# Kernel tuning notes

Measured on AMD Instinct MI355X. Metric: run time of the kernel, lower is better.

The kernel has to match this reference:

```python
import jax, jax.numpy as jnp
import numpy as np

EMBED = 64
TEMPERATURE = 8.0
LN_EPS = 1e-6


def setup_inputs() -> dict:
    key = jax.random.key(0)
    ks = jax.random.split(key, 9)
    n_map, n_obs = 16384, 8192
    s = 1.0 / np.sqrt(EMBED)
    return {
        "map_code": jax.random.normal(ks[0], (n_map, EMBED), jnp.float32),
        "obs_code": jax.random.normal(ks[1], (n_obs, EMBED), jnp.float32),
        "Wq": jax.random.normal(ks[2], (EMBED, EMBED), jnp.float32) * s,
        "Wk": jax.random.normal(ks[3], (EMBED, EMBED), jnp.float32) * s,
        "Wv": jax.random.normal(ks[4], (EMBED, EMBED), jnp.float32) * s,
        "Wo": jax.random.normal(ks[5], (EMBED // 2, EMBED), jnp.float32) * (1.0 / np.sqrt(EMBED // 2)),
        "bo": jnp.zeros((EMBED,), jnp.float32),
        "gamma": jnp.ones((EMBED,), jnp.float32),
        "beta": jnp.zeros((EMBED,), jnp.float32),
    }


def _glu(x):
    a, b = jnp.split(x, 2, axis=-1)
    return a * jax.nn.sigmoid(b)


def reference(map_code, obs_code, Wq, Wk, Wv, Wo, bo, gamma, beta):
    # projections (x @ W == torch Linear with weight W.T; params are random either way)
    map_q = map_code @ Wq          # [Nm, E]
    map_k = map_code @ Wk          # [Nm, E]
    map_v = map_code @ Wv          # [Nm, E]
    obs_k = obs_code @ Wk          # [No, E]
    obs_v = obs_code @ Wv          # [No, E]

    self_score = jnp.sum(map_q * map_k, axis=-1, keepdims=True)   # [Nm, 1]
    obs_score = map_q @ obs_k.T                                   # [Nm, No]
    w = jax.nn.softmax(
        jnp.concatenate([self_score, obs_score], axis=-1) / TEMPERATURE,
        axis=-1,
    )  # [Nm, 1+No]

    # GLU gating: glu(obs_v) is identical for every map row, so the original's
    # [Nm, 1+No, E] broadcast collapses to a rank-2 contraction.
    gated_map = _glu(map_v)   # [Nm, E/2]
    gated_obs = _glu(obs_v)   # [No, E/2]
    agg = w[:, :1] * gated_map + w[:, 1:] @ gated_obs   # [Nm, E/2]

    out = agg @ Wo + bo + map_code   # [Nm, E]
    mu = jnp.mean(out, axis=-1, keepdims=True)
    var = jnp.mean(jnp.square(out - mu), axis=-1, keepdims=True)
    return (out - mu) * jax.lax.rsqrt(var + LN_EPS) * gamma + beta
```

## Files before the change

### kernel.cpp

```cpp
#include <hip/hip_runtime.h>
#include <hip/hip_bf16.h>


typedef float f32x16 __attribute__((ext_vector_type(16)));
typedef short bf16x8 __attribute__((ext_vector_type(8)));
typedef unsigned int u32;

__device__ __forceinline__ u32 cvt_pk_bf16(float lo, float hi) {
    u32 r;
    asm("v_cvt_pk_bf16_f32 %0, %1, %2" : "=v"(r) : "v"(lo), "v"(hi));
    return r;
}
__device__ __forceinline__ void permswap32(u32& a, u32& b) {
    asm("v_permlane32_swap_b32 %0, %1" : "+v"(a), "+v"(b));
}

#define IT 0.18033688011112042f
#define LOG2E 1.44269504089f

__global__ __launch_bounds__(256) void prep_kernel(
    const float* __restrict__ map_code, const float* __restrict__ obs_code,
    const float* __restrict__ Wq, const float* __restrict__ Wk,
    const float* __restrict__ Wv,
    __hip_bfloat16* __restrict__ qbf, __hip_bfloat16* __restrict__ Kp,
    __hip_bfloat16* __restrict__ Vp, float* __restrict__ self_score,
    float* __restrict__ gated_map, int n_map, int n_obs)
{
    __shared__ float xs[32 * 64];
    const int t = threadIdx.x;
    const int w = t >> 6;
    const int e = t & 63;
    const int r0 = blockIdx.x * 32;
    const int total = n_map + n_obs;

    #pragma unroll
    for (int i = 0; i < 8; ++i) {
        const int idx = i * 256 + t;
        const int gr = r0 + (idx >> 6);
        const int col = idx & 63;
        float val = 0.0f;
        if (gr < n_map)      val = map_code[(size_t)gr * 64 + col];
        else if (gr < total) val = obs_code[(size_t)(gr - n_map) * 64 + col];
        xs[idx] = val;
    }
    __syncthreads();

    float qa[8] = {}, ka[8] = {}, va[8] = {};
    const float* xw = xs + (w * 8) * 64;
    for (int d = 0; d < 64; ++d) {
        const float wq = Wq[d * 64 + e];
        const float wk = Wk[d * 64 + e];
        const float wv = Wv[d * 64 + e];
        #pragma unroll
        for (int i = 0; i < 8; ++i) {
            const float x = xw[i * 64 + d];
            qa[i] = fmaf(x, wq, qa[i]);
            ka[i] = fmaf(x, wk, ka[i]);
            va[i] = fmaf(x, wv, va[i]);
        }
    }

    #pragma unroll
    for (int i = 0; i < 8; ++i) {
        const int r = r0 + w * 8 + i;
        if (r >= total) break;
        const bool is_map = r < n_map;
        const float vother = __shfl_xor(va[i], 32);
        const float sig = 1.0f / (1.0f + __builtin_amdgcn_exp2f(-vother * LOG2E));
        const float g = va[i] * sig;

        if (is_map) {
            qbf[(size_t)r * 64 + e] = __float2bfloat16(qa[i] * IT);
            float qk = qa[i] * ka[i];
            #pragma unroll
            for (int off = 32; off; off >>= 1) qk += __shfl_xor(qk, off);
            if (e == 0) self_score[r] = qk;
            if (e < 32) gated_map[(size_t)r * 32 + e] = g;
        } else {
            const int j  = r - n_map;
            const int kb = j >> 5, jq = j & 31;
            {
                const int c = e >> 4, h2 = (e >> 3) & 1, ii = e & 7;
                Kp[(size_t)kb * 2048 + c * 512 + (h2 * 32 + jq) * 8 + ii] =
                    __float2bfloat16(ka[i]);
            }
            if (e < 32) {
                const int h = jq >> 4, h3 = (jq >> 3) & 1, ii = jq & 7;
                Vp[(size_t)kb * 1024 + h * 512 + (h3 * 32 + e) * 8 + ii] =
                    __float2bfloat16(g);
            }
        }
    }
}

#define WAVES 8
__global__ __launch_bounds__(64 * WAVES, 4) void attn_partial(
    const __hip_bfloat16* __restrict__ qbf, const __hip_bfloat16* __restrict__ Kp,
    const __hip_bfloat16* __restrict__ Vp,
    float* __restrict__ oP, float* __restrict__ lP, int n_obs)
{
    const int tid  = threadIdx.x;
    const int w    = tid >> 6;
    const int lane = tid & 63;
    const int ql   = lane & 31;
    const int hi   = lane >> 5;
    const int tile = blockIdx.x >> 1;
    const int half = blockIdx.x & 1;
    const int q    = tile * 32 + ql;

    __shared__ float oL[WAVES][32][33];
    __shared__ float lL[WAVES][32];

    bf16x8 qf[4];
    {
        const __hip_bfloat16* qrow = qbf + (size_t)q * 64 + 8 * hi;
        #pragma unroll
        for (int c = 0; c < 4; ++c)
            qf[c] = *reinterpret_cast<const bf16x8*>(qrow + c * 16);
    }

    float lsumA = 0.0f, lsumB = 0.0f;
    f32x16 o = {};

    const int kb_per_wave = n_obs >> 9;
    const int kb_begin = (half * (n_obs >> 1) + w * (n_obs >> 4)) >> 5;
    const int kb_end   = kb_begin + 16;
    const __hip_bfloat16* Kw = Kp + (size_t)lane * 8;
    const __hip_bfloat16* Vw = Vp + (size_t)lane * 8;
    (void)kb_per_wave;

    auto loadKV = [&](int kb, bf16x8 (&kf)[4], bf16x8 (&vf)[2]) {
        const __hip_bfloat16* kbp = Kw + (size_t)kb * 2048;
        #pragma unroll
        for (int c = 0; c < 4; ++c)
            kf[c] = *reinterpret_cast<const bf16x8*>(kbp + c * 512);
        const __hip_bfloat16* vbp = Vw + (size_t)kb * 1024;
        vf[0] = *reinterpret_cast<const bf16x8*>(vbp);
        vf[1] = *reinterpret_cast<const bf16x8*>(vbp + 512);
    };

    auto body = [&](const bf16x8 (&kf)[4], const bf16x8 (&vf)[2]) {
        f32x16 s = {};
        #pragma unroll
        for (int c = 0; c < 4; ++c)
            s = __builtin_amdgcn_mfma_f32_32x32x16_bf16(kf[c], qf[c], s, 0, 0, 0);
        float p[16];
        #pragma unroll
        for (int r = 0; r < 16; ++r) p[r] = __builtin_amdgcn_exp2f(s[r]);
        #pragma unroll
        for (int r = 0; r < 8; ++r) { lsumA += p[r]; lsumB += p[r + 8]; }
        union { u32 u[4]; bf16x8 v; } pb0, pb1;
        {
            u32 x0 = cvt_pk_bf16(p[0], p[1]);
            u32 x1 = cvt_pk_bf16(p[2], p[3]);
            u32 y0 = cvt_pk_bf16(p[4], p[5]);
            u32 y1 = cvt_pk_bf16(p[6], p[7]);
            permswap32(x0, y0);
            permswap32(x1, y1);
            pb0.u[0] = x0; pb0.u[1] = x1; pb0.u[2] = y0; pb0.u[3] = y1;
        }
        {
            u32 x0 = cvt_pk_bf16(p[8],  p[9]);
            u32 x1 = cvt_pk_bf16(p[10], p[11]);
            u32 y0 = cvt_pk_bf16(p[12], p[13]);
            u32 y1 = cvt_pk_bf16(p[14], p[15]);
            permswap32(x0, y0);
            permswap32(x1, y1);
            pb1.u[0] = x0; pb1.u[1] = x1; pb1.u[2] = y0; pb1.u[3] = y1;
        }
        o = __builtin_amdgcn_mfma_f32_32x32x16_bf16(vf[0], pb0.v, o, 0, 0, 0);
        o = __builtin_amdgcn_mfma_f32_32x32x16_bf16(vf[1], pb1.v, o, 0, 0, 0);
    };

    bf16x8 kA[4], kB[4], vA[2], vB[2];
    loadKV(kb_begin, kA, vA);
    for (int kb = kb_begin; kb < kb_end; kb += 2) {
        loadKV(kb + 1, kB, vB);
        body(kA, vA);
        const int kn = (kb + 2 < kb_end) ? kb + 2 : kb_begin;
        loadKV(kn, kA, vA);
        body(kB, vB);
    }

    float lsum = lsumA + lsumB;
    lsum += __shfl_xor(lsum, 32);
    if (hi == 0) lL[w][ql] = lsum;
    #pragma unroll
    for (int r = 0; r < 16; ++r) {
        const int vr = (r & 3) + 8 * (r >> 2) + 4 * hi;
        oL[w][vr][ql] = o[r];
    }
    __syncthreads();

    if (tid < 32) {
        float l = 0.0f;
        #pragma unroll
        for (int j = 0; j < WAVES; ++j) l += lL[j][tid];
        lP[(size_t)blockIdx.x * 32 + tid] = l;
    }
    #pragma unroll
    for (int t = tid; t < 1024; t += 64 * WAVES) {
        const int v  = t >> 5;
        const int qq = t & 31;
        float a = 0.0f;
        #pragma unroll
        for (int j = 0; j < WAVES; ++j) a += oL[j][v][qq];
        oP[(size_t)blockIdx.x * 1024 + t] = a;
    }
}

__global__ __launch_bounds__(256) void combine_epi(
    const float* __restrict__ oP, const float* __restrict__ lP,
    const float* __restrict__ self_score, const float* __restrict__ gated_map,
    const float* __restrict__ map_code, const float* __restrict__ Wo,
    const float* __restrict__ bo, const float* __restrict__ gamma,
    const float* __restrict__ beta, float* __restrict__ out)
{
    const int tid  = threadIdx.x;
    const int w    = tid >> 6;
    const int lane = tid & 63;
    const int q0   = blockIdx.x * 32;

    __shared__ float aggT[32][33];
    __shared__ float invS[32];
    __shared__ float psS[32];

    if (tid < 32) {
        const float ps = __builtin_amdgcn_exp2f(self_score[q0 + tid] * IT);
        psS[tid] = ps;
        const float l = ps + lP[(size_t)blockIdx.x * 64 + tid]
                           + lP[(size_t)blockIdx.x * 64 + 32 + tid];
        invS[tid] = 1.0f / l;
    }
    __syncthreads();

    const float* oA = oP + (size_t)blockIdx.x * 2048;
    const float* oB = oA + 1024;
    #pragma unroll
    for (int t = tid; t < 1024; t += 256) {
        const int v  = t >> 5;
        const int qq = t & 31;
        aggT[v][qq] = oA[t] + oB[t]
                    + psS[qq] * gated_map[(size_t)(q0 + qq) * 32 + v];
    }
    __syncthreads();

    float wo[32];
    #pragma unroll
    for (int vv = 0; vv < 32; ++vv) wo[vv] = Wo[vv * 64 + lane];
    const float bo_e = bo[lane], ga = gamma[lane], be = beta[lane];

    #pragma unroll
    for (int i = 0; i < 8; ++i) {
        const int qq = w * 8 + i;
        float dot = 0.0f;
        #pragma unroll
        for (int vv = 0; vv < 32; ++vv)
            dot = fmaf(aggT[vv][qq], wo[vv], dot);
        float acc = dot * invS[qq] + bo_e + map_code[(size_t)(q0 + qq) * 64 + lane];
        float mu = acc;
        #pragma unroll
        for (int off = 32; off; off >>= 1) mu += __shfl_xor(mu, off);
        mu *= (1.0f / 64.0f);
        const float dc = acc - mu;
        float var = dc * dc;
        #pragma unroll
        for (int off = 32; off; off >>= 1) var += __shfl_xor(var, off);
        var *= (1.0f / 64.0f);
        out[(size_t)(q0 + qq) * 64 + lane] =
            dc * rsqrtf(var + 1e-6f) * ga + be;
    }
}

extern "C" void kernel_launch(void* const* d_in, const int* in_sizes, int n_in,
                              void* d_out, int out_size, void* d_ws, size_t ws_size,
                              hipStream_t stream) {
    const float* map_code = (const float*)d_in[0];
    const float* obs_code = (const float*)d_in[1];
    const float* Wq  = (const float*)d_in[2];
    const float* Wk  = (const float*)d_in[3];
    const float* Wv  = (const float*)d_in[4];
    const float* Wo  = (const float*)d_in[5];
    const float* bo  = (const float*)d_in[6];
    const float* gam = (const float*)d_in[7];
    const float* bet = (const float*)d_in[8];
    const int n_map = in_sizes[0] / 64;
    const int n_obs = in_sizes[1] / 64;
    const int ntiles = n_map / 32;

    char* ws = (char*)d_ws;
    __hip_bfloat16* qbf = (__hip_bfloat16*)ws; ws += (size_t)n_map * 64 * 2;
    __hip_bfloat16* Kp  = (__hip_bfloat16*)ws; ws += (size_t)n_obs * 64 * 2;
    __hip_bfloat16* Vp  = (__hip_bfloat16*)ws; ws += (size_t)n_obs * 32 * 2;
    float* self_score   = (float*)ws;          ws += (size_t)n_map * 4;
    float* gated_map    = (float*)ws;          ws += (size_t)n_map * 32 * 4;
    float* oP           = (float*)ws;          ws += (size_t)2 * ntiles * 1024 * 4;
    float* lP           = (float*)ws;

    const int total = n_map + n_obs;
    prep_kernel<<<(total + 31) / 32, 256, 0, stream>>>(
        map_code, obs_code, Wq, Wk, Wv, qbf, Kp, Vp, self_score, gated_map,
        n_map, n_obs);
    attn_partial<<<2 * ntiles, 64 * WAVES, 0, stream>>>(
        qbf, Kp, Vp, oP, lP, n_obs);
    combine_epi<<<ntiles, 256, 0, stream>>>(
        oP, lP, self_score, gated_map, map_code, Wo, bo, gam, bet,
        (float*)d_out);
}
```

Measured before the change: 64.97 us.

## Give each wave its own query tile and split keys across blocks

```diff
diff --git a/kernel.cpp b/kernel.cpp
--- a/kernel.cpp
+++ b/kernel.cpp
@@ -47,6 +47,7 @@
 
     float qa[8] = {}, ka[8] = {}, va[8] = {};
     const float* xw = xs + (w * 8) * 64;
+    #pragma unroll 4
     for (int d = 0; d < 64; ++d) {
         const float wq = Wq[d * 64 + e];
         const float wk = Wk[d * 64 + e];
@@ -97,19 +98,19 @@
 __global__ __launch_bounds__(64 * WAVES, 4) void attn_partial(
     const __hip_bfloat16* __restrict__ qbf, const __hip_bfloat16* __restrict__ Kp,
     const __hip_bfloat16* __restrict__ Vp,
-    float* __restrict__ oP, float* __restrict__ lP, int n_obs)
+    float* __restrict__ oP, float* __restrict__ lP,
+    int n_obs, int n_map, int kslog)
 {
     const int tid  = threadIdx.x;
     const int w    = tid >> 6;
     const int lane = tid & 63;
     const int ql   = lane & 31;
     const int hi   = lane >> 5;
-    const int tile = blockIdx.x >> 1;
-    const int half = blockIdx.x & 1;
-    const int q    = tile * 32 + ql;
-
-    __shared__ float oL[WAVES][32][33];
-    __shared__ float lL[WAVES][32];
+    const int ks   = 1 << kslog;
+    const int qb   = blockIdx.x >> kslog;
+    const int slice= blockIdx.x & (ks - 1);
+    const int tileT= qb * WAVES + w;
+    const int q    = tileT * 32 + ql;
 
     bf16x8 qf[4];
     {
@@ -122,12 +123,11 @@
     float lsumA = 0.0f, lsumB = 0.0f;
     f32x16 o = {};
 
-    const int kb_per_wave = n_obs >> 9;
-    const int kb_begin = (half * (n_obs >> 1) + w * (n_obs >> 4)) >> 5;
-    const int kb_end   = kb_begin + 16;
+    const int nkb      = (n_obs >> kslog) >> 5;
+    const int kb_begin = slice * nkb;
+    const int kb_end   = kb_begin + nkb;
     const __hip_bfloat16* Kw = Kp + (size_t)lane * 8;
     const __hip_bfloat16* Vw = Vp + (size_t)lane * 8;
-    (void)kb_per_wave;
 
     auto loadKV = [&](int kb, bf16x8 (&kf)[4], bf16x8 (&vf)[2]) {
         const __hip_bfloat16* kbp = Kw + (size_t)kb * 2048;
@@ -174,38 +174,24 @@
 
     bf16x8 kA[4], kB[4], vA[2], vB[2];
     loadKV(kb_begin, kA, vA);
-    for (int kb = kb_begin; kb < kb_end; kb += 2) {
+    int it = 0;
+    for (int kb = kb_begin; kb < kb_end; kb += 2, ++it) {
         loadKV(kb + 1, kB, vB);
         body(kA, vA);
         const int kn = (kb + 2 < kb_end) ? kb + 2 : kb_begin;
         loadKV(kn, kA, vA);
         body(kB, vB);
+        if ((it & 1) == 1) __syncthreads();
     }
 
     float lsum = lsumA + lsumB;
     lsum += __shfl_xor(lsum, 32);
-    if (hi == 0) lL[w][ql] = lsum;
+    if (hi == 0) lP[(size_t)slice * n_map + tileT * 32 + ql] = lsum;
+    float* ob = oP + ((size_t)slice * (n_map >> 5) + tileT) * 1024;
     #pragma unroll
     for (int r = 0; r < 16; ++r) {
         const int vr = (r & 3) + 8 * (r >> 2) + 4 * hi;
-        oL[w][vr][ql] = o[r];
-    }
-    __syncthreads();
-
-    if (tid < 32) {
-        float l = 0.0f;
-        #pragma unroll
-        for (int j = 0; j < WAVES; ++j) l += lL[j][tid];
-        lP[(size_t)blockIdx.x * 32 + tid] = l;
-    }
-    #pragma unroll
-    for (int t = tid; t < 1024; t += 64 * WAVES) {
-        const int v  = t >> 5;
-        const int qq = t & 31;
-        float a = 0.0f;
-        #pragma unroll
-        for (int j = 0; j < WAVES; ++j) a += oL[j][v][qq];
-        oP[(size_t)blockIdx.x * 1024 + t] = a;
+        ob[vr * 32 + ql] = o[r];
     }
 }
 
@@ -214,12 +200,15 @@
     const float* __restrict__ self_score, const float* __restrict__ gated_map,
     const float* __restrict__ map_code, const float* __restrict__ Wo,
     const float* __restrict__ bo, const float* __restrict__ gamma,
-    const float* __restrict__ beta, float* __restrict__ out)
+    const float* __restrict__ beta, float* __restrict__ out,
+    int n_map, int ks)
 {
     const int tid  = threadIdx.x;
     const int w    = tid >> 6;
     const int lane = tid & 63;
-    const int q0   = blockIdx.x * 32;
+    const int T    = blockIdx.x;
+    const int q0   = T * 32;
+    const int ntiles = n_map >> 5;
 
     __shared__ float aggT[32][33];
     __shared__ float invS[32];
@@ -228,20 +217,21 @@
     if (tid < 32) {
         const float ps = __builtin_amdgcn_exp2f(self_score[q0 + tid] * IT);
         psS[tid] = ps;
-        const float l = ps + lP[(size_t)blockIdx.x * 64 + tid]
-                           + lP[(size_t)blockIdx.x * 64 + 32 + tid];
+        float l = ps;
+        for (int s = 0; s < ks; ++s)
+            l += lP[(size_t)s * n_map + q0 + tid];
         invS[tid] = 1.0f / l;
     }
     __syncthreads();
 
-    const float* oA = oP + (size_t)blockIdx.x * 2048;
-    const float* oB = oA + 1024;
     #pragma unroll
     for (int t = tid; t < 1024; t += 256) {
         const int v  = t >> 5;
         const int qq = t & 31;
-        aggT[v][qq] = oA[t] + oB[t]
-                    + psS[qq] * gated_map[(size_t)(q0 + qq) * 32 + v];
+        float a = psS[qq] * gated_map[(size_t)(q0 + qq) * 32 + v];
+        for (int s = 0; s < ks; ++s)
+            a += oP[((size_t)s * ntiles + T) * 1024 + t];
+        aggT[v][qq] = a;
     }
     __syncthreads();
 
@@ -294,16 +284,22 @@
     __hip_bfloat16* Vp  = (__hip_bfloat16*)ws; ws += (size_t)n_obs * 32 * 2;
     float* self_score   = (float*)ws;          ws += (size_t)n_map * 4;
     float* gated_map    = (float*)ws;          ws += (size_t)n_map * 32 * 4;
-    float* oP           = (float*)ws;          ws += (size_t)2 * ntiles * 1024 * 4;
-    float* lP           = (float*)ws;
+    const size_t base   = (size_t)(ws - (char*)d_ws);
+    const size_t per_slice = (size_t)n_map * 32 * 4 + (size_t)n_map * 4;
+    int kslog = 3;
+    while (kslog > 0 && base + ((size_t)1 << kslog) * per_slice > ws_size)
+        --kslog;
+    const int ks = 1 << kslog;
+    float* oP = (float*)ws;  ws += (size_t)ks * n_map * 32 * 4;
+    float* lP = (float*)ws;
 
     const int total = n_map + n_obs;
     prep_kernel<<<(total + 31) / 32, 256, 0, stream>>>(
         map_code, obs_code, Wq, Wk, Wv, qbf, Kp, Vp, self_score, gated_map,
         n_map, n_obs);
-    attn_partial<<<2 * ntiles, 64 * WAVES, 0, stream>>>(
-        qbf, Kp, Vp, oP, lP, n_obs);
+    attn_partial<<<(n_map / 256) * ks, 64 * WAVES, 0, stream>>>(
+        qbf, Kp, Vp, oP, lP, n_obs, n_map, kslog);
     combine_epi<<<ntiles, 256, 0, stream>>>(
         oP, lP, self_score, gated_map, map_code, Wo, bo, gam, bet,
-        (float*)d_out);
-}
+        (float*)d_out, n_map, ks);
+}
```

Measured after the change: 71.79 us. 10.5% more time.
